# Kernel optimization log

Measured on AMD Instinct MI355X. Metric: run time of the kernel, lower is better.

## Reference

```python
import jax, jax.numpy as jnp
import numpy as np

H = 256                      # latent_channels = LSTM hidden
OC = [32, 64, 64, 128]       # out_channels per mesh level
V = [5023, 1256, 314, 79, 20]  # vertex counts per level (fine -> coarse)
L = 9                        # spiral length
T = 64                       # audio frames (batch for decoder)


def setup_inputs() -> dict:
    key = jax.random.key(0)
    ks = iter(jax.random.split(key, 80))
    f32 = jnp.float32

    def nrm(shape, fan_in):
        return jax.random.normal(next(ks), shape, f32) * (1.0 / np.sqrt(fan_in))

    inp = {}
    inp['audio'] = jax.random.normal(next(ks), (T, 768), f32)
    inp['actor'] = jax.random.normal(next(ks), (V[0], 3), f32)

    # 5-layer bidirectional LSTM; layer 0 input 768, layers 1-4 input 2H
    inp['lstm_Wih0'] = nrm((2, 4 * H, 768), 768)
    inp['lstm_Whh0'] = nrm((2, 4 * H, H), H)
    inp['lstm_b0'] = jnp.zeros((2, 4 * H), f32)
    inp['lstm_Wih'] = nrm((4, 2, 4 * H, 2 * H), 2 * H)
    inp['lstm_Whh'] = nrm((4, 2, 4 * H, H), H)
    inp['lstm_b'] = jnp.zeros((4, 2, 4 * H), f32)

    # decoder entry fc: 2*latent -> num_vert * oc[-1]
    inp['fc_W'] = nrm((V[4] * OC[3], 2 * H), 2 * H)
    inp['fc_b'] = jnp.zeros((V[4] * OC[3],), f32)

    # SpiralConv weights (torch Linear layout: [out, in*L])
    inp['conv3_W'] = nrm((128, 128 * L), 128 * L); inp['conv3_b'] = jnp.zeros((128,), f32)
    inp['conv2_W'] = nrm((64, 128 * L), 128 * L);  inp['conv2_b'] = jnp.zeros((64,), f32)
    inp['conv1_W'] = nrm((64, 64 * L), 64 * L);    inp['conv1_b'] = jnp.zeros((64,), f32)
    inp['conv0_W'] = nrm((32, 64 * L), 64 * L);    inp['conv0_b'] = jnp.zeros((32,), f32)
    inp['head_W'] = nrm((3, 32 * L), 32 * L);      inp['head_b'] = jnp.zeros((3,), f32)

    # spiral indices per level: [V_j, L] with values in [0, V_j)
    for j in range(4):
        inp[f'idx{j}'] = jax.random.randint(next(ks), (V[j], L), 0, V[j], jnp.int32)

    # up_transform[j] sparse [V_j, V_{j+1}], ~3 nnz per row (COO)
    for j in range(4):
        nnz = 3 * V[j]
        inp[f'rows{j}'] = jnp.repeat(jnp.arange(V[j], dtype=jnp.int32), 3)
        inp[f'cols{j}'] = jax.random.randint(next(ks), (nnz,), 0, V[j + 1], jnp.int32)
        inp[f'vals{j}'] = jax.random.uniform(next(ks), (nnz,), f32) / 3.0
    return inp


def _lstm_dir(x, Wih, Whh, b, reverse):
    # x: [T, Din]; torch gate order i, f, g, o
    def step(carry, xt):
        h, c = carry
        g = Wih @ xt + Whh @ h + b            # [4H]
        i, f, gg, o = jnp.split(g, 4)
        c = jax.nn.sigmoid(f) * c + jax.nn.sigmoid(i) * jnp.tanh(gg)
        h = jax.nn.sigmoid(o) * jnp.tanh(c)
        return (h, c), h
    init = (jnp.zeros((H,), x.dtype), jnp.zeros((H,), x.dtype))
    _, hs = jax.lax.scan(step, init, x, reverse=reverse)
    return hs  # [T, H], aligned with input order


def _bilstm(x, Wih, Whh, b):
    hf = _lstm_dir(x, Wih[0], Whh[0], b[0], False)
    hb = _lstm_dir(x, Wih[1], Whh[1], b[1], True)
    return jnp.concatenate([hf, hb], axis=-1)  # [T, 2H]


def _pool(x, rows, cols, vals, n_out):
    # sparse up-transform: out[t, r] = sum_nnz vals * x[t, cols]
    g = x[:, cols, :] * vals[None, :, None]                       # [T, nnz, C]
    return jax.ops.segment_sum(g.swapaxes(0, 1), rows, num_segments=n_out).swapaxes(0, 1)


def _spiral(x, idx, W, b):
    # gather fixed spiral neighborhoods then dense linear
    g = x[:, idx, :].reshape(x.shape[0], idx.shape[0], -1)        # [T, V, L*C]
    return g @ W.T + b


def reference(audio, actor, lstm_Wih0, lstm_Whh0, lstm_b0, lstm_Wih, lstm_Whh, lstm_b,
              fc_W, fc_b, conv3_W, conv3_b, conv2_W, conv2_b, conv1_W, conv1_b,
              conv0_W, conv0_b, head_W, head_b,
              vals3, vals2, vals1, vals0,
              idx0, idx1, idx2, idx3,
              rows3, cols3, rows2, cols2, rows1, cols1, rows0, cols0):
    # audio embedding: 5-layer bidirectional LSTM (batch = 1)
    z = _bilstm(audio, lstm_Wih0, lstm_Whh0, lstm_b0)
    for l in range(4):
        z = _bilstm(z, lstm_Wih[l], lstm_Whh[l], lstm_b[l])       # [T, 2H]

    # decode
    x = (z @ fc_W.T + fc_b).reshape(z.shape[0], V[4], OC[3])      # [T, 20, 128]
    x = jax.nn.elu(_spiral(_pool(x, rows3, cols3, vals3, V[3]), idx3, conv3_W, conv3_b))
    x = jax.nn.elu(_spiral(_pool(x, rows2, cols2, vals2, V[2]), idx2, conv2_W, conv2_b))
    x = jax.nn.elu(_spiral(_pool(x, rows1, cols1, vals1, V[1]), idx1, conv1_W, conv1_b))
    x = jax.nn.elu(_spiral(_pool(x, rows0, cols0, vals0, V[0]), idx0, conv0_W, conv0_b))
    x = _spiral(x, idx0, head_W, head_b)                          # [T, 5023, 3]
    return x + actor[None]
```

## Files before the change

### kernel.cpp

```cpp
#include <hip/hip_runtime.h>
#include <hip/hip_bf16.h>

typedef __attribute__((ext_vector_type(8))) __bf16 bf16x8;
typedef __attribute__((ext_vector_type(4))) float  f32x4;
typedef __attribute__((ext_vector_type(4))) int    i32x4;

#define SCOPE_AGENT __HIP_MEMORY_SCOPE_AGENT

static __device__ __forceinline__ f32x4 mfma16(bf16x8 a, bf16x8 b, f32x4 c) {
    return __builtin_amdgcn_mfma_f32_16x16x32_bf16(a, b, c, 0, 0, 0);
}
static __device__ __forceinline__ i32x4 mfma_i8(i32x4 a, i32x4 b, i32x4 c) {
    return __builtin_amdgcn_mfma_i32_16x16x64_i8(a, b, c, 0, 0, 0);
}
static __device__ __forceinline__ float sigm(float x)  { return 1.0f / (1.0f + __expf(-x)); }
static __device__ __forceinline__ float tanh_(float x) { return 1.0f - 2.0f / (__expf(2.0f * x) + 1.0f); }

static __device__ __forceinline__ bf16x8 cvt8(const float* __restrict__ p) {
    const float4* q = (const float4*)p;
    float4 a = q[0], b = q[1];
    bf16x8 r;
    r[0] = (__bf16)a.x; r[1] = (__bf16)a.y; r[2] = (__bf16)a.z; r[3] = (__bf16)a.w;
    r[4] = (__bf16)b.x; r[5] = (__bf16)b.y; r[6] = (__bf16)b.z; r[7] = (__bf16)b.w;
    return r;
}
static __device__ __forceinline__ void signal_add(unsigned int* p) {
    __hip_atomic_fetch_add(p, 1u, __ATOMIC_RELEASE, SCOPE_AGENT);
}
template <int SLP>
static __device__ __forceinline__ void wait_eq(unsigned int* p, unsigned int v) {
    while (__hip_atomic_load(p, __ATOMIC_RELAXED, SCOPE_AGENT) != v)
        __builtin_amdgcn_s_sleep(SLP);
    (void)__hip_atomic_load(p, __ATOMIC_ACQUIRE, SCOPE_AGENT);
}
union g4u { unsigned long long q; __bf16 h[4]; };

#define ZBUF_OFF   1024
#define GX_OFF     132096
#define CONVW_OFF  66560
#define ARENA_A    621248
#define ARENA_B    21195456
#define WHHQ_BOFF  11534336
#define SWP_BOFF   14155776

__global__ __launch_bounds__(256) void precvt(
    const float* __restrict__ Whh0, const float* __restrict__ WhhL,
    signed char* __restrict__ WhhQ, float* __restrict__ swp,
    const float* __restrict__ fcW, __bf16* __restrict__ fcWb)
{
    if (blockIdx.x >= 2560) {
        int f = ((blockIdx.x - 2560) * 256 + threadIdx.x) * 4;
        if (f < 1310720) {
            float4 v = *(const float4*)(fcW + f);
            g4u u;
            u.h[0] = (__bf16)v.x; u.h[1] = (__bf16)v.y;
            u.h[2] = (__bf16)v.z; u.h[3] = (__bf16)v.w;
            *(unsigned long long*)(fcWb + f) = u.q;
        }
        return;
    }
    const int g  = blockIdx.x * 4 + (threadIdx.x >> 6);
    const int dl = g >> 10;
    const int r  = g & 1023;
    const int lane = threadIdx.x & 63;
    const float* src = (dl < 2 ? Whh0 + (size_t)dl * 262144
                               : WhhL + (size_t)(dl - 2) * 262144) + (size_t)r * 256;
    float4 v = *(const float4*)(src + lane * 4);
    float am = fmaxf(fmaxf(fabsf(v.x), fabsf(v.y)), fmaxf(fabsf(v.z), fabsf(v.w)));
    #pragma unroll
    for (int m = 1; m < 64; m <<= 1) am = fmaxf(am, __shfl_xor(am, m));
    const float inv = am > 0.f ? 127.f / am : 0.f;
    int q0 = __float2int_rn(v.x * inv), q1 = __float2int_rn(v.y * inv);
    int q2 = __float2int_rn(v.z * inv), q3 = __float2int_rn(v.w * inv);
    unsigned pk = (q0 & 255) | ((q1 & 255) << 8) | ((q2 & 255) << 16) | ((q3 & 255) << 24);
    const int gate = r >> 8, cell = r & 255;
    const int m  = cell * 4 + gate;
    const int lm = m & 15, mt = m >> 4;
    const int k  = lane * 4;
    const int kc = k >> 6, qd = (k >> 4) & 3, j = k & 15;
    size_t addr = ((((size_t)dl * 64 + mt) * 4 + kc) * 64 + (qd * 16 + lm)) * 16 + j;
    *(unsigned*)(WhhQ + addr) = pk;
    if (lane == 0) swp[(size_t)dl * 1024 + cell * 4 + gate] = am / 127.f;
}

__global__ __launch_bounds__(512) __attribute__((amdgpu_waves_per_eu(2, 2)))
void lstm_fused(
    const float* __restrict__ audio,
    const float* __restrict__ Wih0,
    const float* __restrict__ WihL,
    const signed char* __restrict__ WhhQ,
    const float* __restrict__ swp,
    const float* __restrict__ b0, const float* __restrict__ bL,
    unsigned short* __restrict__ Gx_g,
    unsigned int* __restrict__ flags,
    unsigned short* __restrict__ zbuf)
{
    const int bid = blockIdx.x;
    const int tid = threadIdx.x;
    const int wave = tid >> 6, lane = tid & 63, ln = lane & 15, quad = lane >> 4;

    __shared__ __align__(16) signed char    hq[2][256];
    __shared__ __align__(16) signed char    zq[4096];
    __shared__ __align__(16) unsigned short gx_l[16384];

    if (bid < 16) {
        const int dir = bid >> 3, sub = bid & 7;
        const int gmt = sub * 8 + wave;
        const int m_a = gmt * 16 + ln;
        const int r_a = (m_a & 3) * 256 + (m_a >> 2);
        unsigned short* GxO = Gx_g + (size_t)dir * 65536;

        {
            const float* Wih_l = Wih0 + (size_t)dir * 786432;
            const float* b_l   = b0 + (size_t)dir * 1024;
            bf16x8 afr[24];
            #pragma unroll
            for (int kc = 0; kc < 24; ++kc)
                afr[kc] = cvt8(Wih_l + (size_t)r_a * 768 + kc * 32 + quad * 8);
            float bv[4];
            #pragma unroll
            for (int reg = 0; reg < 4; ++reg) {
                const int m_row = gmt * 16 + quad * 4 + reg;
                bv[reg] = b_l[(m_row & 3) * 256 + (m_row >> 2)];
            }
            for (int ii = 0; ii < 4; ++ii) {
                const int nt = dir ? 3 - ii : ii;
                const int t  = nt * 16 + ln;
                f32x4 acA = (f32x4){0.f, 0.f, 0.f, 0.f};
                f32x4 acB = (f32x4){0.f, 0.f, 0.f, 0.f};
                #pragma unroll
                for (int kc = 0; kc < 24; kc += 2) {
                    acA = mfma16(afr[kc],
                                 cvt8(audio + (size_t)t * 768 + kc * 32 + quad * 8), acA);
                    acB = mfma16(afr[kc + 1],
                                 cvt8(audio + (size_t)t * 768 + (kc + 1) * 32 + quad * 8), acB);
                }
                f32x4 acc = acA + acB;
                #pragma unroll
                for (int reg = 0; reg < 4; ++reg) {
                    const int m_row = gmt * 16 + quad * 4 + reg;
                    __bf16 v = (__bf16)(acc[reg] + bv[reg]);
                    GxO[(size_t)t * 1024 + m_row] = __builtin_bit_cast(unsigned short, v);
                }
                __syncthreads();
                if (tid == 0) { __threadfence(); signal_add(&flags[(0 * 2 + dir) * 4 + nt]); }
            }
        }

        for (int l = 1; l < 5; ++l) {
            const float* Wih_l = WihL + (size_t)((l - 1) * 2 + dir) * 524288;
            const float* b_l   = bL + (size_t)((l - 1) * 2 + dir) * 1024;
            bf16x8 afr[16];
            #pragma unroll
            for (int kc = 0; kc < 16; ++kc)
                afr[kc] = cvt8(Wih_l + (size_t)r_a * 512 + kc * 32 + quad * 8);
            float bv[4];
            #pragma unroll
            for (int reg = 0; reg < 4; ++reg) {
                const int m_row = gmt * 16 + quad * 4 + reg;
                bv[reg] = b_l[(m_row & 3) * 256 + (m_row >> 2)];
            }
            if (tid == 0) wait_eq<4>(&flags[48 + (l - 1)], 2u);
            __syncthreads();
            const __bf16* zp = (const __bf16*)(zbuf + (size_t)((l - 1) & 1) * 32768);

            for (int ii = 0; ii < 4; ++ii) {
                const int nt = dir ? 3 - ii : ii;
                const int t  = nt * 16 + ln;
                f32x4 acA = (f32x4){0.f, 0.f, 0.f, 0.f};
                f32x4 acB = (f32x4){0.f, 0.f, 0.f, 0.f};
                #pragma unroll
                for (int kc = 0; kc < 16; kc += 2) {
                    acA = mfma16(afr[kc],
                                 *(const bf16x8*)(zp + (size_t)t * 512 + kc * 32 + quad * 8), acA);
                    acB = mfma16(afr[kc + 1],
                                 *(const bf16x8*)(zp + (size_t)t * 512 + (kc + 1) * 32 + quad * 8), acB);
                }
                f32x4 acc = acA + acB;
                #pragma unroll
                for (int reg = 0; reg < 4; ++reg) {
                    const int m_row = gmt * 16 + quad * 4 + reg;
                    __bf16 v = (__bf16)(acc[reg] + bv[reg]);
                    GxO[(size_t)t * 1024 + m_row] = __builtin_bit_cast(unsigned short, v);
                }
                __syncthreads();
                if (tid == 0) { __threadfence(); signal_add(&flags[(l * 2 + dir) * 4 + nt]); }
            }
        }
    } else {
        const int dir = bid - 16;
        const unsigned short* Gx_d = Gx_g + (size_t)dir * 65536;
        const bool owner = (ln < 8);
        const int cell = wave * 32 + ln * 4 + quad;
        const int gcell = owner ? cell : 0;
        const i32x4 czero = (i32x4){0, 0, 0, 0};

        for (int l = 0; l < 5; ++l) {
            const int dl = l * 2 + dir;
            i32x4 wf[8][4];
            const i32x4* wb = (const i32x4*)(WhhQ + (size_t)dl * 262144);
            #pragma unroll
            for (int i = 0; i < 8; ++i)
                #pragma unroll
                for (int kc = 0; kc < 4; ++kc)
                    wf[i][kc] = wb[(size_t)(((wave * 8 + i) * 4 + kc)) * 64 + lane];
            float sc0 = 0.f, sc1 = 0.f, sc2 = 0.f, sc3 = 0.f;
            if (owner) {
                float4 s4 = *(const float4*)(swp + (size_t)dl * 1024 + cell * 4);
                const float f = 1.f / 127.f;
                sc0 = s4.x * f; sc1 = s4.y * f; sc2 = s4.z * f; sc3 = s4.w * f;
            }
            if (tid < 64) ((unsigned int*)hq[0])[tid] = 0;
            float cst = 0.f;
            unsigned short* zl = zbuf + (size_t)(l & 1) * 32768;
            const int gxbase = (l * 2 + dir) * 4;

            for (int blk = 0; blk < 4; ++blk) {
                const int nt = dir ? 3 - blk : blk;
                if (tid == 0) wait_eq<1>(&flags[gxbase + nt], 8u);
                __syncthreads();
                {
                    const float4* src = (const float4*)(Gx_d + (size_t)nt * 16384);
                    float4* dst = (float4*)gx_l;
                    #pragma unroll
                    for (int i = 0; i < 4; ++i) dst[i * 512 + tid] = src[i * 512 + tid];
                }
                __syncthreads();

                for (int ss = 0; ss < 16; ++ss) {
                    const int s = blk * 16 + ss;
                    const int tl = dir ? 15 - ss : ss;
                    const int cur = s & 1, nxt = cur ^ 1;
                    g4u gx;
                    gx.q = *(const unsigned long long*)&gx_l[tl * 1024 + gcell * 4];
                    i32x4 acc[8];
                    {
                        i32x4 b0v = *(const i32x4*)&hq[cur][quad * 16];
                        #pragma unroll
                        for (int i = 0; i < 8; ++i) acc[i] = mfma_i8(wf[i][0], b0v, czero);
                    }
                    #pragma unroll
                    for (int kc = 1; kc < 4; ++kc) {
                        i32x4 b = *(const i32x4*)&hq[cur][kc * 64 + quad * 16];
                        #pragma unroll
                        for (int i = 0; i < 8; ++i) acc[i] = mfma_i8(wf[i][kc], b, acc[i]);
                    }
                    i32x4 a = acc[0];
                    #pragma unroll
                    for (int j = 1; j < 8; ++j) if (ln == j) a = acc[j];
                    if (owner) {
                        float gi = (float)a[0] * sc0 + (float)gx.h[0];
                        float gf = (float)a[1] * sc1 + (float)gx.h[1];
                        float gg = (float)a[2] * sc2 + (float)gx.h[2];
                        float go = (float)a[3] * sc3 + (float)gx.h[3];
                        cst = sigm(gf) * cst + sigm(gi) * tanh_(gg);
                        float h = sigm(go) * tanh_(cst);
                        int q = __float2int_rn(h * 127.f);
                        hq[nxt][cell] = (signed char)q;
                        zq[tl * 256 + cell] = (signed char)q;
                    }
                    __syncthreads();
                }
                #pragma unroll
                for (int i = 0; i < 2; ++i) {
                    const int d = i * 512 + tid;
                    const int tf = d >> 4, cb = (d & 15) * 4;
                    unsigned u = ((const unsigned*)zq)[d];
                    g4u o;
                    #pragma unroll
                    for (int j = 0; j < 4; ++j) {
                        int bch = (int)(signed char)(u >> (8 * j));
                        o.h[j] = (__bf16)((float)bch * (1.f / 127.f));
                    }
                    *(unsigned long long*)(zl + (size_t)(nt * 16 + tf) * 512 + dir * 256 + cb) = o.q;
                }
            }
            if (tid == 0) { __threadfence(); signal_add(&flags[48 + l]); }
        }
    }
}

__global__ __launch_bounds__(256) void fc_kernel(
    const __bf16* __restrict__ zb, const __bf16* __restrict__ W,
    const float* __restrict__ bb, __bf16* __restrict__ out,
    const float* __restrict__ c3W, const float* __restrict__ c2W,
    const float* __restrict__ c1W, const float* __restrict__ c0W,
    const float* __restrict__ hW, __bf16* __restrict__ convWb)
{
    const int tid = threadIdx.x;
    if (blockIdx.x >= 40) {
        int f = ((blockIdx.x - 40) * 256 + tid) * 4;
        if (f < 277344) {
            const float* src; int off;
            if (f < 147456)      { src = c3W; off = f; }
            else if (f < 221184) { src = c2W; off = f - 147456; }
            else if (f < 258048) { src = c1W; off = f - 221184; }
            else if (f < 276480) { src = c0W; off = f - 258048; }
            else                 { src = hW;  off = f - 276480; }
            float4 v = *(const float4*)(src + off);
            g4u u;
            u.h[0] = (__bf16)v.x; u.h[1] = (__bf16)v.y;
            u.h[2] = (__bf16)v.z; u.h[3] = (__bf16)v.w;
            *(unsigned long long*)(convWb + f) = u.q;
        }
        return;
    }
    const int wave = tid >> 6, lane = tid & 63, ln = lane & 15, quad = lane >> 4;
    const int nbase = blockIdx.x * 64;
    f32x4 acc[4];
    #pragma unroll
    for (int nt = 0; nt < 4; nt++) acc[nt] = (f32x4){0.f, 0.f, 0.f, 0.f};
    #pragma unroll 2
    for (int kc = 0; kc < 16; kc++) {
        const int k0 = kc * 32 + quad * 8;
        bf16x8 a = *(const bf16x8*)(zb + (size_t)(wave * 16 + ln) * 512 + k0);
        #pragma unroll
        for (int nt = 0; nt < 4; nt++) {
            bf16x8 b = *(const bf16x8*)(W + (size_t)(nbase + nt * 16 + ln) * 512 + k0);
            acc[nt] = mfma16(a, b, acc[nt]);
        }
    }
    #pragma unroll
    for (int nt = 0; nt < 4; nt++) {
        const int n = nbase + nt * 16 + ln;
        const float bv = bb[n];
        #pragma unroll
        for (int reg = 0; reg < 4; reg++) {
            const int t = wave * 16 + quad * 4 + reg;
            out[(size_t)((n >> 7) * 64 + t) * 128 + (n & 127)] = (__bf16)(acc[nt][reg] + bv);
        }
    }
}

template <int C>
__global__ __launch_bounds__(256) void pool_kernel(
    const __bf16* __restrict__ in, __bf16* __restrict__ out,
    const int* __restrict__ cols, const float* __restrict__ vals, int V)
{
    const int P = 64 * C / 8;
    const int gid = blockIdx.x * 256 + threadIdx.x;
    if (gid >= V * P) return;
    const int r = gid / P;
    const int rem = gid - r * P;
    float acc[8] = {0.f, 0.f, 0.f, 0.f, 0.f, 0.f, 0.f, 0.f};
    #pragma unroll
    for (int s = 0; s < 3; s++) {
        const int col = cols[3 * r + s];
        const float vv = vals[3 * r + s];
        bf16x8 x = *(const bf16x8*)(in + (size_t)col * 64 * C + rem * 8);
        #pragma unroll
        for (int e = 0; e < 8; e++) acc[e] += vv * (float)x[e];
    }
    bf16x8 ov;
    #pragma unroll
    for (int e = 0; e < 8; e++) ov[e] = (__bf16)acc[e];
    *(bf16x8*)(out + (size_t)r * 64 * C + rem * 8) = ov;
}

template <int CIN, int COUT>
__global__ __launch_bounds__(64) void conv_kernel(
    const __bf16* __restrict__ in, __bf16* __restrict__ out,
    const int* __restrict__ idx, const __bf16* __restrict__ W,
    const float* __restrict__ bias)
{
    constexpr int K = 9 * CIN;
    constexpr int NT = COUT / 16;
    constexpr int NKC = K / 32;
    const int v = blockIdx.x;
    const int lane = threadIdx.x, ln = lane & 15, quad = lane >> 4;
    const int t0 = blockIdx.y * 16;
    __shared__ int sIdx[9];
    if (lane < 9) sIdx[lane] = idx[v * 9 + lane];
    __syncthreads();
    f32x4 acc[NT];
    #pragma unroll
    for (int nt = 0; nt < NT; nt++) acc[nt] = (f32x4){0.f, 0.f, 0.f, 0.f};
    const int tt = t0 + ln;
    for (int kc = 0; kc < NKC; kc++) {
        const int k0 = kc * 32;
        const int l = k0 / CIN;
        const int c = (k0 & (CIN - 1)) + quad * 8;
        const int row = sIdx[l];
        bf16x8 a = *(const bf16x8*)(in + ((size_t)row * 64 + tt) * CIN + c);
        #pragma unroll
        for (int nt = 0; nt < NT; nt++) {
            bf16x8 b = *(const bf16x8*)(W + (size_t)(nt * 16 + ln) * K + k0 + quad * 8);
            acc[nt] = mfma16(a, b, acc[nt]);
        }
    }
    #pragma unroll
    for (int nt = 0; nt < NT; nt++) {
        const int n = nt * 16 + ln;
        const float bv = bias[n];
        #pragma unroll
        for (int reg = 0; reg < 4; reg++) {
            const int t = t0 + quad * 4 + reg;
            float val = acc[nt][reg] + bv;
            val = val > 0.f ? val : (__expf(val) - 1.f);
            out[((size_t)v * 64 + t) * COUT + n] = (__bf16)val;
        }
    }
}

__global__ __launch_bounds__(64) void head_kernel(
    const __bf16* __restrict__ in, float* __restrict__ out,
    const int* __restrict__ idx, const __bf16* __restrict__ W,
    const float* __restrict__ bias, const float* __restrict__ actor)
{
    const int v = blockIdx.x;
    const int lane = threadIdx.x, ln = lane & 15, quad = lane >> 4;
    const int t0 = blockIdx.y * 16;
    __shared__ int sIdx[9];
    if (lane < 9) sIdx[lane] = idx[v * 9 + lane];
    __syncthreads();
    f32x4 acc = (f32x4){0.f, 0.f, 0.f, 0.f};
    const int tt = t0 + ln;
    const int rown = ln < 3 ? ln : 0;
    #pragma unroll
    for (int kc = 0; kc < 9; kc++) {
        const int row = sIdx[kc];
        bf16x8 a = *(const bf16x8*)(in + ((size_t)row * 64 + tt) * 32 + quad * 8);
        bf16x8 b = *(const bf16x8*)(W + (size_t)rown * 288 + kc * 32 + quad * 8);
        acc = mfma16(a, b, acc);
    }
    if (ln < 3) {
        const float bv = bias[ln];
        const float av = actor[v * 3 + ln];
        #pragma unroll
        for (int reg = 0; reg < 4; reg++) {
            const int t = t0 + quad * 4 + reg;
            out[((size_t)t * 5023 + v) * 3 + ln] = acc[reg] + bv + av;
        }
    }
}

extern "C" void kernel_launch(void* const* d_in, const int* in_sizes, int n_in,
                              void* d_out, int out_size, void* d_ws, size_t ws_size,
                              hipStream_t stream) {
    const float* audio = (const float*)d_in[0];
    const float* actor = (const float*)d_in[1];
    const float* Wih0  = (const float*)d_in[2];
    const float* Whh0  = (const float*)d_in[3];
    const float* b0    = (const float*)d_in[4];
    const float* WihL  = (const float*)d_in[5];
    const float* WhhL  = (const float*)d_in[6];
    const float* bLs   = (const float*)d_in[7];
    const float* fcW   = (const float*)d_in[8];
    const float* fcb   = (const float*)d_in[9];
    const float* c3W = (const float*)d_in[10]; const float* c3b = (const float*)d_in[11];
    const float* c2W = (const float*)d_in[12]; const float* c2b = (const float*)d_in[13];
    const float* c1W = (const float*)d_in[14]; const float* c1b = (const float*)d_in[15];
    const float* c0W = (const float*)d_in[16]; const float* c0b = (const float*)d_in[17];
    const float* hW  = (const float*)d_in[18]; const float* hb  = (const float*)d_in[19];
    const int* idx0 = (const int*)d_in[20];
    const int* idx1 = (const int*)d_in[21];
    const int* idx2 = (const int*)d_in[22];
    const int* idx3 = (const int*)d_in[23];
    const int* cols0 = (const int*)d_in[25]; const float* vals0 = (const float*)d_in[26];
    const int* cols1 = (const int*)d_in[28]; const float* vals1 = (const float*)d_in[29];
    const int* cols2 = (const int*)d_in[31]; const float* vals2 = (const float*)d_in[32];
    const int* cols3 = (const int*)d_in[34]; const float* vals3 = (const float*)d_in[35];

    char* ws = (char*)d_ws;
    unsigned int*   flags = (unsigned int*)ws;
    unsigned short* zbuf  = (unsigned short*)(ws + ZBUF_OFF);
    unsigned short* GxG   = (unsigned short*)(ws + GX_OFF);
    __bf16*         convWb = (__bf16*)(ws + CONVW_OFF);
    char* arenaA = ws + ARENA_A;
    char* arenaB = ws + ARENA_B;

    signed char* whhq = (signed char*)(arenaB + WHHQ_BOFF);
    float*       swp  = (float*)(arenaB + SWP_BOFF);
    __bf16*      fcWb = (__bf16*)(arenaB + 2097152);

    __bf16* x4b = (__bf16*)arenaA;
    __bf16* p3  = (__bf16*)arenaB;
    __bf16* c3o = (__bf16*)arenaA;
    __bf16* p2  = (__bf16*)arenaB;
    __bf16* c2o = (__bf16*)arenaA;
    __bf16* p1  = (__bf16*)arenaB;
    __bf16* c1o = (__bf16*)arenaA;
    __bf16* p0  = (__bf16*)arenaB;
    __bf16* c0o = (__bf16*)arenaA;

    (void)hipMemsetAsync(ws, 0, 1024, stream);

    precvt<<<3840, 256, 0, stream>>>(Whh0, WhhL, whhq, swp, fcW, fcWb);

    lstm_fused<<<18, 512, 0, stream>>>(audio, Wih0, WihL, whhq, swp, b0, bLs,
                                       GxG, flags, zbuf);

    fc_kernel<<<40 + 271, 256, 0, stream>>>((const __bf16*)zbuf, fcWb, fcb, x4b,
                                            c3W, c2W, c1W, c0W, hW, convWb);

    { int n = 79 * 64 * 128 / 8;
      pool_kernel<128><<<(n + 255) / 256, 256, 0, stream>>>(x4b, p3, cols3, vals3, 79);
      conv_kernel<128, 128><<<dim3(79, 4), 64, 0, stream>>>(p3, c3o, idx3, convWb + 0, c3b); }
    { int n = 314 * 64 * 128 / 8;
      pool_kernel<128><<<(n + 255) / 256, 256, 0, stream>>>(c3o, p2, cols2, vals2, 314);
      conv_kernel<128, 64><<<dim3(314, 4), 64, 0, stream>>>(p2, c2o, idx2, convWb + 147456, c2b); }
    { int n = 1256 * 64 * 64 / 8;
      pool_kernel<64><<<(n + 255) / 256, 256, 0, stream>>>(c2o, p1, cols1, vals1, 1256);
      conv_kernel<64, 64><<<dim3(1256, 4), 64, 0, stream>>>(p1, c1o, idx1, convWb + 221184, c1b); }
    { int n = 5023 * 64 * 64 / 8;
      pool_kernel<64><<<(n + 255) / 256, 256, 0, stream>>>(c1o, p0, cols0, vals0, 5023);
      conv_kernel<64, 32><<<dim3(5023, 4), 64, 0, stream>>>(p0, c0o, idx0, convWb + 258048, c0b); }

    head_kernel<<<dim3(5023, 4), 64, 0, stream>>>(c0o, (float*)d_out, idx0,
                                                  convWb + 276480, hb, actor);
}
```

Before: 818.3 us.

## Fuse decoder fc, pool, conv and head stages into one cooperative kernel

Replaces the ten separate decoder launches (fc, pools, spiral convs, head) with a single cooperative persistent kernel that runs each stage as a grid-stride phase separated by grid-wide barriers. Conv and head now use 256-thread blocks, with four waves covering the 64 time rows of a vertex instead of four separate 64-thread blocks. The goal is to remove per-launch overhead and tail gaps between the many small kernels. In exchange it adds grid-sync cost and a fixed grid size sized from occupancy, which may underfill or serialize the large late stages.

```diff
diff --git a/kernel.cpp b/kernel.cpp
--- a/kernel.cpp
+++ b/kernel.cpp
@@ -1,5 +1,8 @@
 #include <hip/hip_runtime.h>
 #include <hip/hip_bf16.h>
+#include <hip/hip_cooperative_groups.h>
+
+namespace cg = cooperative_groups;
 
 typedef __attribute__((ext_vector_type(8))) __bf16 bf16x8;
 typedef __attribute__((ext_vector_type(4))) float  f32x4;
@@ -280,33 +283,26 @@
     }
 }
 
-__global__ __launch_bounds__(256) void fc_kernel(
-    const __bf16* __restrict__ zb, const __bf16* __restrict__ W,
-    const float* __restrict__ bb, __bf16* __restrict__ out,
-    const float* __restrict__ c3W, const float* __restrict__ c2W,
-    const float* __restrict__ c1W, const float* __restrict__ c0W,
-    const float* __restrict__ hW, __bf16* __restrict__ convWb)
+struct DecArgs {
+    const __bf16* zb; const __bf16* fcWb; const float* fcb;
+    const float* c3W; const float* c2W; const float* c1W; const float* c0W;
+    const float* hW;  __bf16* convWb;
+    __bf16* x4b; __bf16* p3; __bf16* c3o; __bf16* p2; __bf16* c2o;
+    __bf16* p1; __bf16* c1o; __bf16* p0; __bf16* c0o;
+    const int* idx0; const int* idx1; const int* idx2; const int* idx3;
+    const int* cols0; const int* cols1; const int* cols2; const int* cols3;
+    const float* vals0; const float* vals1; const float* vals2; const float* vals3;
+    const float* c3b; const float* c2b; const float* c1b; const float* c0b;
+    const float* hb; const float* actor; float* out;
+};
+
+static __device__ void fc_body(int b, const __bf16* __restrict__ zb,
+                               const __bf16* __restrict__ W,
+                               const float* __restrict__ bb, __bf16* __restrict__ out)
 {
     const int tid = threadIdx.x;
-    if (blockIdx.x >= 40) {
-        int f = ((blockIdx.x - 40) * 256 + tid) * 4;
-        if (f < 277344) {
-            const float* src; int off;
-            if (f < 147456)      { src = c3W; off = f; }
-            else if (f < 221184) { src = c2W; off = f - 147456; }
-            else if (f < 258048) { src = c1W; off = f - 221184; }
-            else if (f < 276480) { src = c0W; off = f - 258048; }
-            else                 { src = hW;  off = f - 276480; }
-            float4 v = *(const float4*)(src + off);
-            g4u u;
-            u.h[0] = (__bf16)v.x; u.h[1] = (__bf16)v.y;
-            u.h[2] = (__bf16)v.z; u.h[3] = (__bf16)v.w;
-            *(unsigned long long*)(convWb + f) = u.q;
-        }
-        return;
-    }
     const int wave = tid >> 6, lane = tid & 63, ln = lane & 15, quad = lane >> 4;
-    const int nbase = blockIdx.x * 64;
+    const int nbase = b * 64;
     f32x4 acc[4];
     #pragma unroll
     for (int nt = 0; nt < 4; nt++) acc[nt] = (f32x4){0.f, 0.f, 0.f, 0.f};
@@ -316,8 +312,8 @@
         bf16x8 a = *(const bf16x8*)(zb + (size_t)(wave * 16 + ln) * 512 + k0);
         #pragma unroll
         for (int nt = 0; nt < 4; nt++) {
-            bf16x8 b = *(const bf16x8*)(W + (size_t)(nbase + nt * 16 + ln) * 512 + k0);
-            acc[nt] = mfma16(a, b, acc[nt]);
+            bf16x8 bfr = *(const bf16x8*)(W + (size_t)(nbase + nt * 16 + ln) * 512 + k0);
+            acc[nt] = mfma16(a, bfr, acc[nt]);
         }
     }
     #pragma unroll
@@ -333,105 +329,161 @@
 }
 
 template <int C>
-__global__ __launch_bounds__(256) void pool_kernel(
-    const __bf16* __restrict__ in, __bf16* __restrict__ out,
-    const int* __restrict__ cols, const float* __restrict__ vals, int V)
+static __device__ void pool_phase(const __bf16* __restrict__ in,
+                                  __bf16* __restrict__ out,
+                                  const int* __restrict__ cols,
+                                  const float* __restrict__ vals, int V)
 {
     const int P = 64 * C / 8;
-    const int gid = blockIdx.x * 256 + threadIdx.x;
-    if (gid >= V * P) return;
-    const int r = gid / P;
-    const int rem = gid - r * P;
-    float acc[8] = {0.f, 0.f, 0.f, 0.f, 0.f, 0.f, 0.f, 0.f};
-    #pragma unroll
-    for (int s = 0; s < 3; s++) {
-        const int col = cols[3 * r + s];
-        const float vv = vals[3 * r + s];
-        bf16x8 x = *(const bf16x8*)(in + (size_t)col * 64 * C + rem * 8);
-        #pragma unroll
-        for (int e = 0; e < 8; e++) acc[e] += vv * (float)x[e];
-    }
-    bf16x8 ov;
-    #pragma unroll
-    for (int e = 0; e < 8; e++) ov[e] = (__bf16)acc[e];
-    *(bf16x8*)(out + (size_t)r * 64 * C + rem * 8) = ov;
+    const int stride = gridDim.x * 256;
+    for (int gid = blockIdx.x * 256 + threadIdx.x; gid < V * P; gid += stride) {
+        const int r = gid / P;
+        const int rem = gid - r * P;
+        float acc[8] = {0.f, 0.f, 0.f, 0.f, 0.f, 0.f, 0.f, 0.f};
+        #pragma unroll
+        for (int s = 0; s < 3; s++) {
+            const int col = cols[3 * r + s];
+            const float vv = vals[3 * r + s];
+            bf16x8 x = *(const bf16x8*)(in + (size_t)col * 64 * C + rem * 8);
+            #pragma unroll
+            for (int e = 0; e < 8; e++) acc[e] += vv * (float)x[e];
+        }
+        bf16x8 ov;
+        #pragma unroll
+        for (int e = 0; e < 8; e++) ov[e] = (__bf16)acc[e];
+        *(bf16x8*)(out + (size_t)r * 64 * C + rem * 8) = ov;
+    }
 }
 
 template <int CIN, int COUT>
-__global__ __launch_bounds__(64) void conv_kernel(
-    const __bf16* __restrict__ in, __bf16* __restrict__ out,
-    const int* __restrict__ idx, const __bf16* __restrict__ W,
-    const float* __restrict__ bias)
+static __device__ void conv_phase(const __bf16* __restrict__ in,
+                                  __bf16* __restrict__ out,
+                                  const int* __restrict__ idx,
+                                  const __bf16* __restrict__ W,
+                                  const float* __restrict__ bias, int V)
 {
     constexpr int K = 9 * CIN;
     constexpr int NT = COUT / 16;
     constexpr int NKC = K / 32;
-    const int v = blockIdx.x;
-    const int lane = threadIdx.x, ln = lane & 15, quad = lane >> 4;
-    const int t0 = blockIdx.y * 16;
+    const int tid = threadIdx.x;
+    const int wave = tid >> 6, lane = tid & 63, ln = lane & 15, quad = lane >> 4;
     __shared__ int sIdx[9];
-    if (lane < 9) sIdx[lane] = idx[v * 9 + lane];
-    __syncthreads();
-    f32x4 acc[NT];
-    #pragma unroll
-    for (int nt = 0; nt < NT; nt++) acc[nt] = (f32x4){0.f, 0.f, 0.f, 0.f};
-    const int tt = t0 + ln;
-    for (int kc = 0; kc < NKC; kc++) {
-        const int k0 = kc * 32;
-        const int l = k0 / CIN;
-        const int c = (k0 & (CIN - 1)) + quad * 8;
-        const int row = sIdx[l];
-        bf16x8 a = *(const bf16x8*)(in + ((size_t)row * 64 + tt) * CIN + c);
+    for (int v = blockIdx.x; v < V; v += gridDim.x) {
+        __syncthreads();
+        if (tid < 9) sIdx[tid] = idx[v * 9 + tid];
+        __syncthreads();
+        f32x4 acc[NT];
+        #pragma unroll
+        for (int nt = 0; nt < NT; nt++) acc[nt] = (f32x4){0.f, 0.f, 0.f, 0.f};
+        const int tt = wave * 16 + ln;
+        for (int kc = 0; kc < NKC; kc++) {
+            const int k0 = kc * 32;
+            const int l = k0 / CIN;
+            const int c = (k0 & (CIN - 1)) + quad * 8;
+            const int row = sIdx[l];
+            bf16x8 a = *(const bf16x8*)(in + ((size_t)row * 64 + tt) * CIN + c);
+            #pragma unroll
+            for (int nt = 0; nt < NT; nt++) {
+                bf16x8 b = *(const bf16x8*)(W + (size_t)(nt * 16 + ln) * K + k0 + quad * 8);
+                acc[nt] = mfma16(a, b, acc[nt]);
+            }
+        }
         #pragma unroll
         for (int nt = 0; nt < NT; nt++) {
-            bf16x8 b = *(const bf16x8*)(W + (size_t)(nt * 16 + ln) * K + k0 + quad * 8);
-            acc[nt] = mfma16(a, b, acc[nt]);
-        }
-    }
-    #pragma unroll
-    for (int nt = 0; nt < NT; nt++) {
-        const int n = nt * 16 + ln;
-        const float bv = bias[n];
-        #pragma unroll
-        for (int reg = 0; reg < 4; reg++) {
-            const int t = t0 + quad * 4 + reg;
-            float val = acc[nt][reg] + bv;
-            val = val > 0.f ? val : (__expf(val) - 1.f);
-            out[((size_t)v * 64 + t) * COUT + n] = (__bf16)val;
-        }
-    }
-}
-
-__global__ __launch_bounds__(64) void head_kernel(
-    const __bf16* __restrict__ in, float* __restrict__ out,
-    const int* __restrict__ idx, const __bf16* __restrict__ W,
-    const float* __restrict__ bias, const float* __restrict__ actor)
-{
-    const int v = blockIdx.x;
-    const int lane = threadIdx.x, ln = lane & 15, quad = lane >> 4;
-    const int t0 = blockIdx.y * 16;
+            const int n = nt * 16 + ln;
+            const float bv = bias[n];
+            #pragma unroll
+            for (int reg = 0; reg < 4; reg++) {
+                const int t = wave * 16 + quad * 4 + reg;
+                float val = acc[nt][reg] + bv;
+                val = val > 0.f ? val : (__expf(val) - 1.f);
+                out[((size_t)v * 64 + t) * COUT + n] = (__bf16)val;
+            }
+        }
+    }
+}
+
+static __device__ void head_phase(const __bf16* __restrict__ in,
+                                  float* __restrict__ out,
+                                  const int* __restrict__ idx,
+                                  const __bf16* __restrict__ W,
+                                  const float* __restrict__ bias,
+                                  const float* __restrict__ actor)
+{
+    const int tid = threadIdx.x;
+    const int wave = tid >> 6, lane = tid & 63, ln = lane & 15, quad = lane >> 4;
     __shared__ int sIdx[9];
-    if (lane < 9) sIdx[lane] = idx[v * 9 + lane];
-    __syncthreads();
-    f32x4 acc = (f32x4){0.f, 0.f, 0.f, 0.f};
-    const int tt = t0 + ln;
-    const int rown = ln < 3 ? ln : 0;
-    #pragma unroll
-    for (int kc = 0; kc < 9; kc++) {
-        const int row = sIdx[kc];
-        bf16x8 a = *(const bf16x8*)(in + ((size_t)row * 64 + tt) * 32 + quad * 8);
-        bf16x8 b = *(const bf16x8*)(W + (size_t)rown * 288 + kc * 32 + quad * 8);
-        acc = mfma16(a, b, acc);
-    }
-    if (ln < 3) {
-        const float bv = bias[ln];
-        const float av = actor[v * 3 + ln];
-        #pragma unroll
-        for (int reg = 0; reg < 4; reg++) {
-            const int t = t0 + quad * 4 + reg;
-            out[((size_t)t * 5023 + v) * 3 + ln] = acc[reg] + bv + av;
-        }
-    }
+    for (int v = blockIdx.x; v < 5023; v += gridDim.x) {
+        __syncthreads();
+        if (tid < 9) sIdx[tid] = idx[v * 9 + tid];
+        __syncthreads();
+        f32x4 acc = (f32x4){0.f, 0.f, 0.f, 0.f};
+        const int tt = wave * 16 + ln;
+        const int rown = ln < 3 ? ln : 0;
+        #pragma unroll
+        for (int kc = 0; kc < 9; kc++) {
+            const int row = sIdx[kc];
+            bf16x8 a = *(const bf16x8*)(in + ((size_t)row * 64 + tt) * 32 + quad * 8);
+            bf16x8 b = *(const bf16x8*)(W + (size_t)rown * 288 + kc * 32 + quad * 8);
+            acc = mfma16(a, b, acc);
+        }
+        if (ln < 3) {
+            const float bv = bias[ln];
+            const float av = actor[v * 3 + ln];
+            #pragma unroll
+            for (int reg = 0; reg < 4; reg++) {
+                const int t = wave * 16 + quad * 4 + reg;
+                out[((size_t)t * 5023 + v) * 3 + ln] = acc[reg] + bv + av;
+            }
+        }
+    }
+}
+
+static __device__ __forceinline__ void gsync() {
+    __threadfence();
+    cg::this_grid().sync();
+}
+
+__global__ __launch_bounds__(256, 4) void decoder_coop(DecArgs a)
+{
+    const int tid = threadIdx.x;
+    for (int b = blockIdx.x; b < 40; b += gridDim.x)
+        fc_body(b, a.zb, a.fcWb, a.fcb, a.x4b);
+    {
+        const int stride = gridDim.x * 256;
+        for (int i = blockIdx.x * 256 + tid; i * 4 < 277344; i += stride) {
+            int f = i * 4;
+            const float* src; int off;
+            if (f < 147456)      { src = a.c3W; off = f; }
+            else if (f < 221184) { src = a.c2W; off = f - 147456; }
+            else if (f < 258048) { src = a.c1W; off = f - 221184; }
+            else if (f < 276480) { src = a.c0W; off = f - 258048; }
+            else                 { src = a.hW;  off = f - 276480; }
+            float4 v = *(const float4*)(src + off);
+            g4u u;
+            u.h[0] = (__bf16)v.x; u.h[1] = (__bf16)v.y;
+            u.h[2] = (__bf16)v.z; u.h[3] = (__bf16)v.w;
+            *(unsigned long long*)(a.convWb + f) = u.q;
+        }
+    }
+    gsync();
+    pool_phase<128>(a.x4b, a.p3, a.cols3, a.vals3, 79);
+    gsync();
+    conv_phase<128, 128>(a.p3, a.c3o, a.idx3, a.convWb + 0, a.c3b, 79);
+    gsync();
+    pool_phase<128>(a.c3o, a.p2, a.cols2, a.vals2, 314);
+    gsync();
+    conv_phase<128, 64>(a.p2, a.c2o, a.idx2, a.convWb + 147456, a.c2b, 314);
+    gsync();
+    pool_phase<64>(a.c2o, a.p1, a.cols1, a.vals1, 1256);
+    gsync();
+    conv_phase<64, 64>(a.p1, a.c1o, a.idx1, a.convWb + 221184, a.c1b, 1256);
+    gsync();
+    pool_phase<64>(a.c1o, a.p0, a.cols0, a.vals0, 5023);
+    gsync();
+    conv_phase<64, 32>(a.p0, a.c0o, a.idx0, a.convWb + 258048, a.c0b, 5023);
+    gsync();
+    head_phase(a.c0o, a.out, a.idx0, a.convWb + 276480, a.hb, a.actor);
 }
 
 extern "C" void kernel_launch(void* const* d_in, const int* in_sizes, int n_in,
@@ -490,22 +542,25 @@
     lstm_fused<<<18, 512, 0, stream>>>(audio, Wih0, WihL, whhq, swp, b0, bLs,
                                        GxG, flags, zbuf);
 
-    fc_kernel<<<40 + 271, 256, 0, stream>>>((const __bf16*)zbuf, fcWb, fcb, x4b,
-                                            c3W, c2W, c1W, c0W, hW, convWb);
-
-    { int n = 79 * 64 * 128 / 8;
-      pool_kernel<128><<<(n + 255) / 256, 256, 0, stream>>>(x4b, p3, cols3, vals3, 79);
-      conv_kernel<128, 128><<<dim3(79, 4), 64, 0, stream>>>(p3, c3o, idx3, convWb + 0, c3b); }
-    { int n = 314 * 64 * 128 / 8;
-      pool_kernel<128><<<(n + 255) / 256, 256, 0, stream>>>(c3o, p2, cols2, vals2, 314);
-      conv_kernel<128, 64><<<dim3(314, 4), 64, 0, stream>>>(p2, c2o, idx2, convWb + 147456, c2b); }
-    { int n = 1256 * 64 * 64 / 8;
-      pool_kernel<64><<<(n + 255) / 256, 256, 0, stream>>>(c2o, p1, cols1, vals1, 1256);
-      conv_kernel<64, 64><<<dim3(1256, 4), 64, 0, stream>>>(p1, c1o, idx1, convWb + 221184, c1b); }
-    { int n = 5023 * 64 * 64 / 8;
-      pool_kernel<64><<<(n + 255) / 256, 256, 0, stream>>>(c1o, p0, cols0, vals0, 5023);
-      conv_kernel<64, 32><<<dim3(5023, 4), 64, 0, stream>>>(p0, c0o, idx0, convWb + 258048, c0b); }
-
-    head_kernel<<<dim3(5023, 4), 64, 0, stream>>>(c0o, (float*)d_out, idx0,
-                                                  convWb + 276480, hb, actor);
-}
+    DecArgs da;
+    da.zb = (const __bf16*)zbuf; da.fcWb = fcWb; da.fcb = fcb;
+    da.c3W = c3W; da.c2W = c2W; da.c1W = c1W; da.c0W = c0W; da.hW = hW;
+    da.convWb = convWb;
+    da.x4b = x4b; da.p3 = p3; da.c3o = c3o; da.p2 = p2; da.c2o = c2o;
+    da.p1 = p1; da.c1o = c1o; da.p0 = p0; da.c0o = c0o;
+    da.idx0 = idx0; da.idx1 = idx1; da.idx2 = idx2; da.idx3 = idx3;
+    da.cols0 = cols0; da.cols1 = cols1; da.cols2 = cols2; da.cols3 = cols3;
+    da.vals0 = vals0; da.vals1 = vals1; da.vals2 = vals2; da.vals3 = vals3;
+    da.c3b = c3b; da.c2b = c2b; da.c1b = c1b; da.c0b = c0b;
+    da.hb = hb; da.actor = actor; da.out = (float*)d_out;
+
+    int nbpc = 0;
+    if (hipOccupancyMaxActiveBlocksPerMultiprocessor(&nbpc, decoder_coop, 256, 0)
+            != hipSuccess || nbpc <= 0) nbpc = 4;
+    if (nbpc > 8) nbpc = 8;
+    int dgrid = nbpc * 256;
+
+    void* kargs[] = { &da };
+    (void)hipLaunchCooperativeKernel((void*)decoder_coop, dim3(dgrid), dim3(256),
+                                     kargs, 0, stream);
+}
```

Result: slower. 1.824 ms (+123.0%).
